# Optimization experiments

Hardware: AMD Instinct MI355X
Metric: run time of the kernel (lower is better)

The kernel has to match this reference:

```python
import jax, jax.numpy as jnp
import numpy as np

SR = 48000          # sample_rate
N = 480000          # num_samples
MAX_DELAYS = 50     # max_num_delays


def one_pole_lowpass(x, a):
    # y[n] = a*x[n] + (1-a)*y[n-1], zero initial state (causal one-pole IIR)
    def step(y, xn):
        y = a * xn + (1.0 - a) * y
        return y, y
    _, ys = jax.lax.scan(step, jnp.zeros((), x.dtype), x)
    return ys


def one_pole_bandpass(x, low, high):
    # bandpass as difference of two one-pole lowpasses (high cutoff minus low cutoff)
    return one_pole_lowpass(x, high) - one_pole_lowpass(x, low)


def setup_inputs() -> dict:
    key = jax.random.key(0)
    k1, k2, k3 = jax.random.split(key, 3)
    input_signal = jax.random.normal(k1, (N,), dtype=jnp.float32)
    parameters = jax.random.uniform(k2, (5,), dtype=jnp.float32)
    delay_buffer = jax.random.normal(k3, (N,), dtype=jnp.float32)
    return {"input_signal": input_signal, "parameters": parameters, "delay_buffer": delay_buffer}


def reference(input_signal, parameters, delay_buffer):
    frequency = jnp.clip(parameters[0], 20.0, SR / 2)
    feedback = jnp.clip(parameters[1], 0.0, 0.99)
    filter_low = jnp.clip(parameters[2], 1e-7, 0.99)
    filter_high = jnp.clip(parameters[3], 1e-7, 0.99)
    gain = jnp.maximum(parameters[4], 1e-7)

    delay_length = jnp.clip(jnp.floor(SR / frequency), 1, N // 2).astype(jnp.int32)
    num_delays = jnp.minimum(N // delay_length, MAX_DELAYS)

    taps = jnp.arange(1, MAX_DELAYS, dtype=jnp.int32)          # i = 1..49
    shifts = taps * delay_length                                # delay_start per tap
    powers = feedback ** taps.astype(jnp.float32)               # feedback^i
    active = (taps < num_delays) & (shifts < N)                 # loop bounds / break mask

    # The one-pole bandpass is linear and causal, so filtering the truncated,
    # scaled segment equals scaling + truncating the filtered full buffer.
    filtered = one_pole_bandpass(delay_buffer, filter_low, filter_high)  # [N]

    rolled = jax.vmap(lambda s: jnp.roll(filtered, s))(shifts)  # [49, N]
    pos = jnp.arange(N)
    valid = (pos[None, :] >= shifts[:, None]) & active[:, None]
    contrib = jnp.where(valid, rolled * powers[:, None], 0.0)   # [49, N]

    output_signal = input_signal + contrib.sum(axis=0)
    return jnp.tanh(output_signal * gain)
```

## Files before the change

kernel.cpp:

```cpp
#include <hip/hip_runtime.h>
#include <math.h>

#define SRATE 48000
#define NN    480000
#define MAXD  50
#define CHUNK 32
#define TPB   256
#define NBLK  59
#define NTHR  (NBLK * TPB)

__device__ __forceinline__ float clampf(float v, float lo, float hi) {
    return fminf(fmaxf(v, lo), hi);
}

struct Params { float al, bl, ah, bh, feedback, gain; int dl, nd; };

__device__ __forceinline__ Params load_params(const float* __restrict__ p) {
    Params q;
    float freq  = clampf(p[0], 20.0f, (float)(SRATE / 2));
    q.feedback  = clampf(p[1], 0.0f, 0.99f);
    float alow  = clampf(p[2], 1e-7f, 0.99f);
    float ahigh = clampf(p[3], 1e-7f, 0.99f);
    q.gain      = fmaxf(p[4], 1e-7f);
    float dlf   = clampf(floorf((float)SRATE / freq), 1.0f, (float)(NN / 2));
    q.dl = (int)dlf;
    q.nd = min(NN / q.dl, MAXD);
    q.al = alow;  q.bl = 1.0f - alow;
    q.ah = ahigh; q.bh = 1.0f - ahigh;
    return q;
}

__global__ __launch_bounds__(TPB) void scan_phase1(
    const float* __restrict__ x, const float* __restrict__ p,
    float* __restrict__ thrYl, float* __restrict__ thrDl,
    float* __restrict__ thrYh, float* __restrict__ thrDh,
    float* __restrict__ blkYl, float* __restrict__ blkDl,
    float* __restrict__ blkYh, float* __restrict__ blkDh)
{
    Params q = load_params(p);
    int tid = threadIdx.x;
    int t = blockIdx.x * TPB + tid;
    int start = t * CHUNK;
    int len = NN - start; len = (len < 0) ? 0 : ((len > CHUNK) ? CHUNK : len);

    float yl = 0.f, yh = 0.f, dl = 1.f, dh = 1.f;
    for (int j = 0; j < len; ++j) {
        float xv = x[start + j];
        yl = fmaf(q.bl, yl, q.al * xv);
        yh = fmaf(q.bh, yh, q.ah * xv);
        dl *= q.bl; dh *= q.bh;
    }

    __shared__ float sYl[TPB], sDl[TPB], sYh[TPB], sDh[TPB];
    sYl[tid] = yl; sDl[tid] = dl; sYh[tid] = yh; sDh[tid] = dh;
    __syncthreads();
    for (int off = 1; off < TPB; off <<= 1) {
        float cYl = sYl[tid], cDl = sDl[tid], cYh = sYh[tid], cDh = sDh[tid];
        float pYl = 0.f, pDl = 1.f, pYh = 0.f, pDh = 1.f;
        bool has = (tid >= off);
        if (has) { pYl = sYl[tid - off]; pDl = sDl[tid - off];
                   pYh = sYh[tid - off]; pDh = sDh[tid - off]; }
        __syncthreads();
        if (has) {
            sYl[tid] = fmaf(cDl, pYl, cYl); sDl[tid] = cDl * pDl;
            sYh[tid] = fmaf(cDh, pYh, cYh); sDh[tid] = cDh * pDh;
        }
        __syncthreads();
    }

    float eYl = 0.f, eDl = 1.f, eYh = 0.f, eDh = 1.f;
    if (tid > 0) { eYl = sYl[tid-1]; eDl = sDl[tid-1];
                   eYh = sYh[tid-1]; eDh = sDh[tid-1]; }
    thrYl[t] = eYl; thrDl[t] = eDl; thrYh[t] = eYh; thrDh[t] = eDh;

    if (tid == TPB - 1) {
        blkYl[blockIdx.x] = sYl[tid]; blkDl[blockIdx.x] = sDl[tid];
        blkYh[blockIdx.x] = sYh[tid]; blkDh[blockIdx.x] = sDh[tid];
    }
}

__global__ __launch_bounds__(TPB) void scan_phase2(
    const float* __restrict__ x, const float* __restrict__ p,
    const float* __restrict__ thrYl, const float* __restrict__ thrDl,
    const float* __restrict__ thrYh, const float* __restrict__ thrDh,
    const float* __restrict__ blkYl, const float* __restrict__ blkDl,
    const float* __restrict__ blkYh, const float* __restrict__ blkDh,
    float* __restrict__ filtered)
{
    Params q = load_params(p);
    __shared__ float sCl, sCh;
    int tid = threadIdx.x;

    if (tid < 64) {
        int l = tid;
        float Yl = (l < NBLK) ? blkYl[l] : 0.f;
        float Dl = (l < NBLK) ? blkDl[l] : 1.f;
        float Yh = (l < NBLK) ? blkYh[l] : 0.f;
        float Dh = (l < NBLK) ? blkDh[l] : 1.f;
        for (int off = 1; off < 64; off <<= 1) {
            float pYl = __shfl_up(Yl, off);
            float pDl = __shfl_up(Dl, off);
            float pYh = __shfl_up(Yh, off);
            float pDh = __shfl_up(Dh, off);
            if (l >= off) {
                Yl = fmaf(Dl, pYl, Yl); Dl *= pDl;
                Yh = fmaf(Dh, pYh, Yh); Dh *= pDh;
            }
        }
        int b = blockIdx.x;
        int src = (b == 0) ? 0 : (b - 1);
        float selYl = __shfl(Yl, src);
        float selYh = __shfl(Yh, src);
        if (l == 0) {
            sCl = (b == 0) ? 0.f : selYl;
            sCh = (b == 0) ? 0.f : selYh;
        }
    }
    __syncthreads();

    int t = blockIdx.x * TPB + tid;
    float yl = fmaf(thrDl[t], sCl, thrYl[t]);
    float yh = fmaf(thrDh[t], sCh, thrYh[t]);
    int start = t * CHUNK;
    int len = NN - start; len = (len < 0) ? 0 : ((len > CHUNK) ? CHUNK : len);
    for (int j = 0; j < len; ++j) {
        float xv = x[start + j];
        yl = fmaf(q.bl, yl, q.al * xv);
        yh = fmaf(q.bh, yh, q.ah * xv);
        filtered[start + j] = yh - yl;
    }
}

__global__ __launch_bounds__(TPB) void taps_kernel(
    const float* __restrict__ input, const float* __restrict__ p,
    const float* __restrict__ filtered, float* __restrict__ out)
{
    int n = blockIdx.x * TPB + threadIdx.x;
    if (n >= NN) return;
    Params q = load_params(p);
    float acc = input[n];
    int s = q.dl;
    float w = q.feedback;
    for (int i = 1; i < q.nd; ++i) {
        if (s > n) break;
        acc = fmaf(w, filtered[n - s], acc);
        s += q.dl;
        w *= q.feedback;
    }
    out[n] = tanhf(acc * q.gain);
}

extern "C" void kernel_launch(void* const* d_in, const int* in_sizes, int n_in,
                              void* d_out, int out_size, void* d_ws, size_t ws_size,
                              hipStream_t stream)
{
    const float* input  = (const float*)d_in[0];
    const float* params = (const float*)d_in[1];
    const float* dbuf   = (const float*)d_in[2];
    float* out = (float*)d_out;

    float* ws       = (float*)d_ws;
    float* filtered = ws;
    float* thrYl = ws + NN;
    float* thrDl = thrYl + NTHR;
    float* thrYh = thrDl + NTHR;
    float* thrDh = thrYh + NTHR;
    float* blkYl = thrDh + NTHR;
    float* blkDl = blkYl + NBLK;
    float* blkYh = blkDl + NBLK;
    float* blkDh = blkYh + NBLK;

    scan_phase1<<<NBLK, TPB, 0, stream>>>(dbuf, params,
        thrYl, thrDl, thrYh, thrDh, blkYl, blkDl, blkYh, blkDh);
    scan_phase2<<<NBLK, TPB, 0, stream>>>(dbuf, params,
        thrYl, thrDl, thrYh, thrDh, blkYl, blkDl, blkYh, blkDh, filtered);
    taps_kernel<<<(NN + TPB - 1) / TPB, TPB, 0, stream>>>(input, params, filtered, out);
}
```

Before: 89.93 us.

## Restructure IIR scan to 4 elements per thread with wave-shuffle scans

Replaces the two-phase chunked scan (59 blocks, 32 sequential elements per thread, with per-thread carries written to global memory) by a reduce-then-scan over float4 segments. The first kernel writes only per-block aggregates, and the second kernel rescans the block aggregates in shared memory and applies the prefix within the block. This spreads the work over about 469 blocks with short serial chains and uses wave shuffles instead of shared-memory sweeps, removing the latency-bound serial loops and the per-thread carry traffic. The tap loop also precomputes its trip count in place of an early break. In exchange, every block repeats the scan over the aggregates, and the longer multiplicative prefix chains may change float rounding slightly.

```diff
diff --git a/kernel.cpp b/kernel.cpp
--- a/kernel.cpp
+++ b/kernel.cpp
@@ -4,10 +4,10 @@
 #define SRATE 48000
 #define NN    480000
 #define MAXD  50
-#define CHUNK 32
 #define TPB   256
-#define NBLK  59
-#define NTHR  (NBLK * TPB)
+#define NV4   (NN / 4)
+#define NBLKS ((NV4 + TPB - 1) / TPB)
+#define NTAPB (NN / TPB)
 
 __device__ __forceinline__ float clampf(float v, float lo, float hi) {
     return fminf(fmaxf(v, lo), hi);
@@ -30,104 +30,146 @@
     return q;
 }
 
-__global__ __launch_bounds__(TPB) void scan_phase1(
+__device__ __forceinline__ void seg_affine(const float4& v, float a, float b,
+                                           float& Y, float& D) {
+    float t = v.x;
+    t = fmaf(t, b, v.y);
+    t = fmaf(t, b, v.z);
+    t = fmaf(t, b, v.w);
+    Y = a * t;
+    float b2 = b * b;
+    D = b2 * b2;
+}
+
+__device__ __forceinline__ void wave_scan(int lane, float& Yl, float& Dl,
+                                          float& Yh, float& Dh) {
+    for (int off = 1; off < 64; off <<= 1) {
+        float pYl = __shfl_up(Yl, off), pDl = __shfl_up(Dl, off);
+        float pYh = __shfl_up(Yh, off), pDh = __shfl_up(Dh, off);
+        if (lane >= off) {
+            Yl = fmaf(Dl, pYl, Yl); Dl *= pDl;
+            Yh = fmaf(Dh, pYh, Yh); Dh *= pDh;
+        }
+    }
+}
+
+__global__ __launch_bounds__(TPB) void scan_agg(
     const float* __restrict__ x, const float* __restrict__ p,
-    float* __restrict__ thrYl, float* __restrict__ thrDl,
-    float* __restrict__ thrYh, float* __restrict__ thrDh,
-    float* __restrict__ blkYl, float* __restrict__ blkDl,
-    float* __restrict__ blkYh, float* __restrict__ blkDh)
+    float4* __restrict__ blkAgg)
 {
     Params q = load_params(p);
     int tid = threadIdx.x;
     int t = blockIdx.x * TPB + tid;
-    int start = t * CHUNK;
-    int len = NN - start; len = (len < 0) ? 0 : ((len > CHUNK) ? CHUNK : len);
-
-    float yl = 0.f, yh = 0.f, dl = 1.f, dh = 1.f;
-    for (int j = 0; j < len; ++j) {
-        float xv = x[start + j];
-        yl = fmaf(q.bl, yl, q.al * xv);
-        yh = fmaf(q.bh, yh, q.ah * xv);
-        dl *= q.bl; dh *= q.bh;
-    }
+    float Yl = 0.f, Dl = 1.f, Yh = 0.f, Dh = 1.f;
+    if (t < NV4) {
+        float4 v = ((const float4*)x)[t];
+        seg_affine(v, q.al, q.bl, Yl, Dl);
+        seg_affine(v, q.ah, q.bh, Yh, Dh);
+    }
+    int lane = tid & 63;
+    wave_scan(lane, Yl, Dl, Yh, Dh);
+
+    __shared__ float wYl[4], wDl[4], wYh[4], wDh[4];
+    int w = tid >> 6;
+    if (lane == 63) { wYl[w] = Yl; wDl[w] = Dl; wYh[w] = Yh; wDh[w] = Dh; }
+    __syncthreads();
+    if (tid == TPB - 1) {
+        float cYl = 0.f, cDl = 1.f, cYh = 0.f, cDh = 1.f;
+        for (int j = 0; j < 3; ++j) {
+            cYl = fmaf(wDl[j], cYl, wYl[j]); cDl *= wDl[j];
+            cYh = fmaf(wDh[j], cYh, wYh[j]); cDh *= wDh[j];
+        }
+        float AYl = fmaf(Dl, cYl, Yl), ADl = Dl * cDl;
+        float AYh = fmaf(Dh, cYh, Yh), ADh = Dh * cDh;
+        blkAgg[blockIdx.x] = make_float4(AYl, ADl, AYh, ADh);
+    }
+}
+
+__global__ __launch_bounds__(TPB) void scan_apply(
+    const float* __restrict__ x, const float* __restrict__ p,
+    const float4* __restrict__ blkAgg,
+    float* __restrict__ filtered)
+{
+    Params q = load_params(p);
+    int tid = threadIdx.x;
+    int lane = tid & 63;
+    int w = tid >> 6;
+    int t = blockIdx.x * TPB + tid;
+    bool valid = (t < NV4);
+
+    float4 v = make_float4(0.f, 0.f, 0.f, 0.f);
+    float Yl = 0.f, Dl = 1.f, Yh = 0.f, Dh = 1.f;
+    if (valid) {
+        v = ((const float4*)x)[t];
+        seg_affine(v, q.al, q.bl, Yl, Dl);
+        seg_affine(v, q.ah, q.bh, Yh, Dh);
+    }
+    wave_scan(lane, Yl, Dl, Yh, Dh);
+
+    __shared__ float wYl[4], wDl[4], wYh[4], wDh[4];
+    if (lane == 63) { wYl[w] = Yl; wDl[w] = Dl; wYh[w] = Yh; wDh[w] = Dh; }
 
     __shared__ float sYl[TPB], sDl[TPB], sYh[TPB], sDh[TPB];
-    sYl[tid] = yl; sDl[tid] = dl; sYh[tid] = yh; sDh[tid] = dh;
+    {
+        int i2 = 2 * tid;
+        float4 a0 = (i2     < NBLKS) ? blkAgg[i2]     : make_float4(0.f, 1.f, 0.f, 1.f);
+        float4 a1 = (i2 + 1 < NBLKS) ? blkAgg[i2 + 1] : make_float4(0.f, 1.f, 0.f, 1.f);
+        sYl[tid] = fmaf(a1.y, a0.x, a1.x); sDl[tid] = a1.y * a0.y;
+        sYh[tid] = fmaf(a1.w, a0.z, a1.z); sDh[tid] = a1.w * a0.w;
+    }
     __syncthreads();
     for (int off = 1; off < TPB; off <<= 1) {
-        float cYl = sYl[tid], cDl = sDl[tid], cYh = sYh[tid], cDh = sDh[tid];
-        float pYl = 0.f, pDl = 1.f, pYh = 0.f, pDh = 1.f;
+        float cyl = sYl[tid], cdl = sDl[tid], cyh = sYh[tid], cdh = sDh[tid];
+        float pyl = 0.f, pdl = 1.f, pyh = 0.f, pdh = 1.f;
         bool has = (tid >= off);
-        if (has) { pYl = sYl[tid - off]; pDl = sDl[tid - off];
-                   pYh = sYh[tid - off]; pDh = sDh[tid - off]; }
+        if (has) { pyl = sYl[tid-off]; pdl = sDl[tid-off];
+                   pyh = sYh[tid-off]; pdh = sDh[tid-off]; }
         __syncthreads();
         if (has) {
-            sYl[tid] = fmaf(cDl, pYl, cYl); sDl[tid] = cDl * pDl;
-            sYh[tid] = fmaf(cDh, pYh, cYh); sDh[tid] = cDh * pDh;
+            sYl[tid] = fmaf(cdl, pyl, cyl); sDl[tid] = cdl * pdl;
+            sYh[tid] = fmaf(cdh, pyh, cyh); sDh[tid] = cdh * pdh;
         }
         __syncthreads();
     }
-
-    float eYl = 0.f, eDl = 1.f, eYh = 0.f, eDh = 1.f;
-    if (tid > 0) { eYl = sYl[tid-1]; eDl = sDl[tid-1];
-                   eYh = sYh[tid-1]; eDh = sDh[tid-1]; }
-    thrYl[t] = eYl; thrDl[t] = eDl; thrYh[t] = eYh; thrDh[t] = eDh;
-
-    if (tid == TPB - 1) {
-        blkYl[blockIdx.x] = sYl[tid]; blkDl[blockIdx.x] = sDl[tid];
-        blkYh[blockIdx.x] = sYh[tid]; blkDh[blockIdx.x] = sDh[tid];
-    }
-}
-
-__global__ __launch_bounds__(TPB) void scan_phase2(
-    const float* __restrict__ x, const float* __restrict__ p,
-    const float* __restrict__ thrYl, const float* __restrict__ thrDl,
-    const float* __restrict__ thrYh, const float* __restrict__ thrDh,
-    const float* __restrict__ blkYl, const float* __restrict__ blkDl,
-    const float* __restrict__ blkYh, const float* __restrict__ blkDh,
-    float* __restrict__ filtered)
-{
-    Params q = load_params(p);
-    __shared__ float sCl, sCh;
-    int tid = threadIdx.x;
-
-    if (tid < 64) {
-        int l = tid;
-        float Yl = (l < NBLK) ? blkYl[l] : 0.f;
-        float Dl = (l < NBLK) ? blkDl[l] : 1.f;
-        float Yh = (l < NBLK) ? blkYh[l] : 0.f;
-        float Dh = (l < NBLK) ? blkDh[l] : 1.f;
-        for (int off = 1; off < 64; off <<= 1) {
-            float pYl = __shfl_up(Yl, off);
-            float pDl = __shfl_up(Dl, off);
-            float pYh = __shfl_up(Yh, off);
-            float pDh = __shfl_up(Dh, off);
-            if (l >= off) {
-                Yl = fmaf(Dl, pYl, Yl); Dl *= pDl;
-                Yh = fmaf(Dh, pYh, Yh); Dh *= pDh;
-            }
-        }
+    __shared__ float GYl_s, GYh_s;
+    if (tid == 0) {
         int b = blockIdx.x;
-        int src = (b == 0) ? 0 : (b - 1);
-        float selYl = __shfl(Yl, src);
-        float selYh = __shfl(Yh, src);
-        if (l == 0) {
-            sCl = (b == 0) ? 0.f : selYl;
-            sCh = (b == 0) ? 0.f : selYh;
-        }
+        int qq = b >> 1;
+        float GYl = 0.f, GDl = 1.f, GYh = 0.f, GDh = 1.f;
+        if (qq > 0) { GYl = sYl[qq-1]; GDl = sDl[qq-1];
+                      GYh = sYh[qq-1]; GDh = sDh[qq-1]; }
+        if (b & 1) {
+            float4 am = blkAgg[2 * qq];
+            GYl = fmaf(am.y, GYl, am.x); GDl = am.y * GDl;
+            GYh = fmaf(am.w, GYh, am.z); GDh = am.w * GDh;
+        }
+        (void)GDl; (void)GDh;
+        GYl_s = GYl; GYh_s = GYh;
     }
     __syncthreads();
 
-    int t = blockIdx.x * TPB + tid;
-    float yl = fmaf(thrDl[t], sCl, thrYl[t]);
-    float yh = fmaf(thrDh[t], sCh, thrYh[t]);
-    int start = t * CHUNK;
-    int len = NN - start; len = (len < 0) ? 0 : ((len > CHUNK) ? CHUNK : len);
-    for (int j = 0; j < len; ++j) {
-        float xv = x[start + j];
-        yl = fmaf(q.bl, yl, q.al * xv);
-        yh = fmaf(q.bh, yh, q.ah * xv);
-        filtered[start + j] = yh - yl;
+    float eYl = __shfl_up(Yl, 1), eDl = __shfl_up(Dl, 1);
+    float eYh = __shfl_up(Yh, 1), eDh = __shfl_up(Dh, 1);
+    if (lane == 0) { eYl = 0.f; eDl = 1.f; eYh = 0.f; eDh = 1.f; }
+    float cYl = 0.f, cDl = 1.f, cYh = 0.f, cDh = 1.f;
+    for (int j = 0; j < 3; ++j) {
+        if (j < w) {
+            cYl = fmaf(wDl[j], cYl, wYl[j]); cDl *= wDl[j];
+            cYh = fmaf(wDh[j], cYh, wYh[j]); cDh *= wDh[j];
+        }
+    }
+    float BYl = fmaf(eDl, cYl, eYl), BDl = eDl * cDl;
+    float BYh = fmaf(eDh, cYh, eYh), BDh = eDh * cDh;
+    float yl = fmaf(BDl, GYl_s, BYl);
+    float yh = fmaf(BDh, GYh_s, BYh);
+
+    if (valid) {
+        float4 o;
+        yl = fmaf(q.bl, yl, q.al * v.x); yh = fmaf(q.bh, yh, q.ah * v.x); o.x = yh - yl;
+        yl = fmaf(q.bl, yl, q.al * v.y); yh = fmaf(q.bh, yh, q.ah * v.y); o.y = yh - yl;
+        yl = fmaf(q.bl, yl, q.al * v.z); yh = fmaf(q.bh, yh, q.ah * v.z); o.z = yh - yl;
+        yl = fmaf(q.bl, yl, q.al * v.w); yh = fmaf(q.bh, yh, q.ah * v.w); o.w = yh - yl;
+        ((float4*)filtered)[t] = o;
     }
 }
 
@@ -139,10 +181,10 @@
     if (n >= NN) return;
     Params q = load_params(p);
     float acc = input[n];
+    int m = min(q.nd - 1, n / q.dl);
     int s = q.dl;
     float w = q.feedback;
-    for (int i = 1; i < q.nd; ++i) {
-        if (s > n) break;
+    for (int i = 1; i <= m; ++i) {
         acc = fmaf(w, filtered[n - s], acc);
         s += q.dl;
         w *= q.feedback;
@@ -161,18 +203,9 @@
 
     float* ws       = (float*)d_ws;
     float* filtered = ws;
-    float* thrYl = ws + NN;
-    float* thrDl = thrYl + NTHR;
-    float* thrYh = thrDl + NTHR;
-    float* thrDh = thrYh + NTHR;
-    float* blkYl = thrDh + NTHR;
-    float* blkDl = blkYl + NBLK;
-    float* blkYh = blkDl + NBLK;
-    float* blkDh = blkYh + NBLK;
-
-    scan_phase1<<<NBLK, TPB, 0, stream>>>(dbuf, params,
-        thrYl, thrDl, thrYh, thrDh, blkYl, blkDl, blkYh, blkDh);
-    scan_phase2<<<NBLK, TPB, 0, stream>>>(dbuf, params,
-        thrYl, thrDl, thrYh, thrDh, blkYl, blkDl, blkYh, blkDh, filtered);
-    taps_kernel<<<(NN + TPB - 1) / TPB, TPB, 0, stream>>>(input, params, filtered, out);
-}
+    float4* blkAgg  = (float4*)(ws + NN);
+
+    scan_agg  <<<NBLKS, TPB, 0, stream>>>(dbuf, params, blkAgg);
+    scan_apply<<<NBLKS, TPB, 0, stream>>>(dbuf, params, blkAgg, filtered);
+    taps_kernel<<<NTAPB, TPB, 0, stream>>>(input, params, filtered, out);
+}
```

After: 76.70 us. 14.7% less time.
